# Kernel optimization log

Hardware: AMD Instinct MI355X
Metric: run time of the kernel (lower is better)

The kernel has to match this reference:

```python
import jax, jax.numpy as jnp
import numpy as np

D = 512      # model dim
H = 8        # heads
HD = D // H  # head dim = 64
NQ = 2048    # n_query
NC = 4096    # n_context
EPS = 1e-5   # LayerNorm eps (torch default)


def setup_inputs() -> dict:
    key = jax.random.key(0)
    ks = jax.random.split(key, 12)
    s = 0.02
    return {
        "query_repr": jax.random.normal(ks[0], (NQ, D), dtype=jnp.float32),
        "context_repr": jax.random.normal(ks[1], (NC, D), dtype=jnp.float32),
        "query_coords": jax.random.uniform(ks[2], (NQ, 2), dtype=jnp.float32) * 10.0,
        "context_coords": jax.random.uniform(ks[3], (NC, 2), dtype=jnp.float32) * 10.0,
        "Wq": jax.random.normal(ks[4], (D, D), dtype=jnp.float32) * s,
        "bq": jnp.zeros((D,), jnp.float32),
        "Wk": jax.random.normal(ks[5], (D, D), dtype=jnp.float32) * s,
        "bk": jnp.zeros((D,), jnp.float32),
        "Wv": jax.random.normal(ks[6], (D, D), dtype=jnp.float32) * s,
        "bv": jnp.zeros((D,), jnp.float32),
        "Wo": jax.random.normal(ks[7], (D, D), dtype=jnp.float32) * s,
        "bo": jnp.zeros((D,), jnp.float32),
        "ln_g": jnp.ones((D,), jnp.float32),
        "ln_b": jnp.zeros((D,), jnp.float32),
        "log_scale": jnp.array(0.0, jnp.float32),          # log_distance_scale
        "bias_per_head": jnp.ones((H,), jnp.float32),      # distance_bias_per_head
    }


def reference(query_repr, context_repr, query_coords, context_coords,
              Wq, bq, Wk, bk, Wv, bv, Wo, bo, ln_g, ln_b,
              log_scale, bias_per_head):
    # pairwise Euclidean distances (NQ, NC)
    diff = query_coords[:, None, :] - context_coords[None, :, :]
    dist = jnp.sqrt(jnp.sum(diff * diff, axis=-1))
    # per-head additive attention bias (H, NQ, NC)
    bias = (-jnp.exp(log_scale) * dist)[None, :, :] * bias_per_head[:, None, None]

    # multi-head attention (batch=1, eval mode so dropout is identity)
    q = (query_repr @ Wq.T + bq).reshape(NQ, H, HD).transpose(1, 0, 2)    # (H, NQ, HD)
    k = (context_repr @ Wk.T + bk).reshape(NC, H, HD).transpose(1, 0, 2)  # (H, NC, HD)
    v = (context_repr @ Wv.T + bv).reshape(NC, H, HD).transpose(1, 0, 2)  # (H, NC, HD)

    scale = 1.0 / jnp.sqrt(jnp.float32(HD))
    scores = jnp.einsum('hqd,hkd->hqk', q, k) * scale + bias              # (H, NQ, NC)
    attn = jax.nn.softmax(scores, axis=-1)
    ctx = jnp.einsum('hqk,hkd->hqd', attn, v)                             # (H, NQ, HD)
    attended = ctx.transpose(1, 0, 2).reshape(NQ, D) @ Wo.T + bo          # (NQ, D)

    # residual + LayerNorm
    x = attended + query_repr
    mu = jnp.mean(x, axis=-1, keepdims=True)
    var = jnp.mean((x - mu) ** 2, axis=-1, keepdims=True)
    return (x - mu) / jnp.sqrt(var + EPS) * ln_g + ln_b
```

## Files before the change

### kernel.cpp

```cpp
#include <hip/hip_runtime.h>

#define D 512
#define H 8
#define HD 64
#define NQ 2048
#define NC 4096
#define SPLIT 8
#define CLEN (NC / SPLIT)
#define NT (CLEN / 32)
#define M0 3.0f
#define KP2 136
#define VP 40

typedef __attribute__((ext_vector_type(8))) short short8;
typedef __attribute__((ext_vector_type(4))) short short4v;
typedef __attribute__((ext_vector_type(4))) float float4v;
typedef __attribute__((ext_vector_type(4))) int int4v;

__device__ inline float bf2f(short s) {
    unsigned int u = ((unsigned int)(unsigned short)s) << 16;
    return __builtin_bit_cast(float, u);
}
__device__ inline short f2bf(float f) {
    unsigned int u = __builtin_bit_cast(unsigned int, f);
    u = (u + 0x7FFF + ((u >> 16) & 1)) >> 16;
    return (short)u;
}
__device__ inline int cvtpk(float a, float b) {
    int w;
    asm("v_cvt_pk_bf16_f32 %0, %1, %2" : "=v"(w) : "v"(a), "v"(b));
    return w;
}

__global__ __launch_bounds__(256) void cast_all(
    const float* __restrict__ s0, const float* __restrict__ s1,
    const float* __restrict__ s2, const float* __restrict__ s3,
    const float* __restrict__ s4, const float* __restrict__ s5,
    short* __restrict__ dst)
{
    int i = blockIdx.x * 256 + threadIdx.x;
    const float* src; int off;
    if      (i < 262144) { src = s0; off = i; }
    else if (i < 786432) { src = s1; off = i - 262144; }
    else if (i < 851968) { src = s2; off = i - 786432; }
    else if (i < 917504) { src = s3; off = i - 851968; }
    else if (i < 983040) { src = s4; off = i - 917504; }
    else                 { src = s5; off = i - 983040; }
    float4v v = ((const float4v*)src)[off];
    short4v o;
    o.x = f2bf(v.x); o.y = f2bf(v.y); o.z = f2bf(v.z); o.w = f2bf(v.w);
    ((short4v*)dst)[i] = o;
}

__global__ __launch_bounds__(256) void gemm_bt_bias(
    const short* __restrict__ X, const short* __restrict__ W,
    const float* __restrict__ bias, short* __restrict__ out, int M)
{
    int wave = threadIdx.x >> 6, lane = threadIdx.x & 63;
    int gt = blockIdx.x * 4 + wave;
    int tm = gt >> 3;
    int tg = gt & 7;
    if (tm >= (M >> 4)) return;
    int l15 = lane & 15, quad = lane >> 4;
    const short* xp = X + (tm * 16 + l15) * D + quad * 8;
    const short* wp = W + (tg * 64 + l15) * D + quad * 8;
    float4v a0 = {0,0,0,0}, a1 = {0,0,0,0}, a2 = {0,0,0,0}, a3 = {0,0,0,0};
#pragma unroll
    for (int k = 0; k < D; k += 32) {
        short8 a  = *(const short8*)(xp + k);
        short8 b0 = *(const short8*)(wp + k);
        short8 b1 = *(const short8*)(wp + 16 * D + k);
        short8 b2 = *(const short8*)(wp + 32 * D + k);
        short8 b3 = *(const short8*)(wp + 48 * D + k);
        a0 = __builtin_amdgcn_mfma_f32_16x16x32_bf16(a, b0, a0, 0, 0, 0);
        a1 = __builtin_amdgcn_mfma_f32_16x16x32_bf16(a, b1, a1, 0, 0, 0);
        a2 = __builtin_amdgcn_mfma_f32_16x16x32_bf16(a, b2, a2, 0, 0, 0);
        a3 = __builtin_amdgcn_mfma_f32_16x16x32_bf16(a, b3, a3, 0, 0, 0);
    }
    int orow = tm * 16 + quad * 4;
    float4v accs[4] = {a0, a1, a2, a3};
#pragma unroll
    for (int j = 0; j < 4; j++) {
        int col = tg * 64 + j * 16 + l15;
        float bv = bias[col];
#pragma unroll
        for (int r = 0; r < 4; r++)
            out[(orow + r) * D + col] = f2bf(accs[j][r] + bv);
    }
}

__global__ __launch_bounds__(256) void gemm_bt_bias_kv(
    const short* __restrict__ X, const short* __restrict__ Wk,
    const short* __restrict__ Wv, const float* __restrict__ bk,
    const float* __restrict__ bv, short* __restrict__ outK,
    short* __restrict__ outVT, int M)
{
    int wave = threadIdx.x >> 6, lane = threadIdx.x & 63;
    int gt = blockIdx.x * 4 + wave;
    int tm = gt >> 3;
    int tg = gt & 7;
    if (tm >= (M >> 4)) return;
    int l15 = lane & 15, quad = lane >> 4;
    const short* xp  = X  + (tm * 16 + l15) * D + quad * 8;
    const short* wkp = Wk + (tg * 64 + l15) * D + quad * 8;
    const short* wvp = Wv + (tg * 64 + l15) * D + quad * 8;
    float4v k0 = {0,0,0,0}, k1 = {0,0,0,0}, k2 = {0,0,0,0}, k3 = {0,0,0,0};
    float4v v0 = {0,0,0,0}, v1 = {0,0,0,0}, v2 = {0,0,0,0}, v3 = {0,0,0,0};
#pragma unroll
    for (int k = 0; k < D; k += 32) {
        short8 a   = *(const short8*)(xp + k);
        short8 bk0 = *(const short8*)(wkp + k);
        short8 bk1 = *(const short8*)(wkp + 16 * D + k);
        short8 bk2 = *(const short8*)(wkp + 32 * D + k);
        short8 bk3 = *(const short8*)(wkp + 48 * D + k);
        short8 bv0 = *(const short8*)(wvp + k);
        short8 bv1 = *(const short8*)(wvp + 16 * D + k);
        short8 bv2 = *(const short8*)(wvp + 32 * D + k);
        short8 bv3 = *(const short8*)(wvp + 48 * D + k);
        k0 = __builtin_amdgcn_mfma_f32_16x16x32_bf16(a, bk0, k0, 0, 0, 0);
        k1 = __builtin_amdgcn_mfma_f32_16x16x32_bf16(a, bk1, k1, 0, 0, 0);
        k2 = __builtin_amdgcn_mfma_f32_16x16x32_bf16(a, bk2, k2, 0, 0, 0);
        k3 = __builtin_amdgcn_mfma_f32_16x16x32_bf16(a, bk3, k3, 0, 0, 0);
        v0 = __builtin_amdgcn_mfma_f32_16x16x32_bf16(a, bv0, v0, 0, 0, 0);
        v1 = __builtin_amdgcn_mfma_f32_16x16x32_bf16(a, bv1, v1, 0, 0, 0);
        v2 = __builtin_amdgcn_mfma_f32_16x16x32_bf16(a, bv2, v2, 0, 0, 0);
        v3 = __builtin_amdgcn_mfma_f32_16x16x32_bf16(a, bv3, v3, 0, 0, 0);
    }
    int orow = tm * 16 + quad * 4;
    {
        float4v accs[4] = {k0, k1, k2, k3};
#pragma unroll
        for (int j = 0; j < 4; j++) {
            int col = tg * 64 + j * 16 + l15;
            float bb = bk[col];
#pragma unroll
            for (int r = 0; r < 4; r++)
                outK[(orow + r) * D + col] = f2bf(accs[j][r] + bb);
        }
    }
    {
        int a = (orow & 31) >> 2;
        int posb = (a < 4) ? (8 * a) : (8 * (a - 4) + 4);
        int cp = (orow & ~31) + posb;
        float4v accs[4] = {v0, v1, v2, v3};
#pragma unroll
        for (int j = 0; j < 4; j++) {
            int col = tg * 64 + j * 16 + l15;
            float bb = bv[col];
            short4v o;
#pragma unroll
            for (int r = 0; r < 4; r++) o[r] = f2bf(accs[j][r] + bb);
            *(short4v*)(outVT + (size_t)col * M + cp) = o;
        }
    }
}

__global__ __launch_bounds__(256) void gemm_bt_bias_res_f32(
    const short* __restrict__ X, const short* __restrict__ W,
    const float* __restrict__ bias, const float* __restrict__ resid,
    float* __restrict__ out, int M)
{
    int wave = threadIdx.x >> 6, lane = threadIdx.x & 63;
    int gt = blockIdx.x * 4 + wave;
    int tm = gt >> 3;
    int tg = gt & 7;
    if (tm >= (M >> 4)) return;
    int l15 = lane & 15, quad = lane >> 4;
    const short* xp = X + (tm * 16 + l15) * D + quad * 8;
    const short* wp = W + (tg * 64 + l15) * D + quad * 8;
    float4v a0 = {0,0,0,0}, a1 = {0,0,0,0}, a2 = {0,0,0,0}, a3 = {0,0,0,0};
#pragma unroll
    for (int k = 0; k < D; k += 32) {
        short8 a  = *(const short8*)(xp + k);
        short8 b0 = *(const short8*)(wp + k);
        short8 b1 = *(const short8*)(wp + 16 * D + k);
        short8 b2 = *(const short8*)(wp + 32 * D + k);
        short8 b3 = *(const short8*)(wp + 48 * D + k);
        a0 = __builtin_amdgcn_mfma_f32_16x16x32_bf16(a, b0, a0, 0, 0, 0);
        a1 = __builtin_amdgcn_mfma_f32_16x16x32_bf16(a, b1, a1, 0, 0, 0);
        a2 = __builtin_amdgcn_mfma_f32_16x16x32_bf16(a, b2, a2, 0, 0, 0);
        a3 = __builtin_amdgcn_mfma_f32_16x16x32_bf16(a, b3, a3, 0, 0, 0);
    }
    int orow = tm * 16 + quad * 4;
    float4v accs[4] = {a0, a1, a2, a3};
#pragma unroll
    for (int j = 0; j < 4; j++) {
        int col = tg * 64 + j * 16 + l15;
        float bv = bias[col];
#pragma unroll
        for (int r = 0; r < 4; r++) {
            int q = orow + r;
            out[q * D + col] = accs[j][r] + bv + resid[q * D + col];
        }
    }
}

__global__ __launch_bounds__(256) void attn_mfma_split9(
    const short* __restrict__ Q, const short* __restrict__ K,
    const short* __restrict__ Vp,
    const float* __restrict__ qc, const float* __restrict__ cc,
    const float* __restrict__ log_scale, const float* __restrict__ bph,
    short* __restrict__ Opart, float* __restrict__ Lpart)
{
    __shared__ __align__(16) short Klds[2][32 * KP2];
    __shared__ __align__(16) short Vlds[2][128 * VP];
    __shared__ __align__(16) float ccl[512];

    int tid = threadIdx.x;
    int wave = tid >> 6, lane = tid & 63;
    int h0 = blockIdx.y * 2;
    int sp = blockIdx.z;
    int q0 = blockIdx.x * 64 + wave * 16;
    int quad = lane >> 4, l15 = lane & 15;
    int cbase = sp * CLEN;

    const float LOG2E = 1.4426950408889634f;
    const float escale = 0.125f * LOG2E;
    const float M0L = M0 * LOG2E;
    float ebase = __expf(log_scale[0]);
    float bh0 = ebase * bph[h0] * LOG2E;
    float bh1 = ebase * bph[h0 + 1] * LOG2E;

    const short* qp = Q + (q0 + l15) * D + h0 * HD + quad * 8;
    short8 qa0_0 = *(const short8*)(qp);
    short8 qa1_0 = *(const short8*)(qp + 32);
    short8 qa0_1 = *(const short8*)(qp + 64);
    short8 qa1_1 = *(const short8*)(qp + 96);

    float qx = qc[(q0 + l15) * 2];
    float qy = qc[(q0 + l15) * 2 + 1];

    float lacc0 = 0.f, lacc1 = 0.f;
    float4v O00 = {0,0,0,0}, O01 = {0,0,0,0}, O02 = {0,0,0,0}, O03 = {0,0,0,0};
    float4v O10 = {0,0,0,0}, O11 = {0,0,0,0}, O12 = {0,0,0,0}, O13 = {0,0,0,0};

    int kr_ = tid >> 3, kc_ = tid & 7;
    int vr_ = tid >> 2, vc_ = tid & 3;
    const short* kg  = K + (size_t)h0 * HD + kc_ * 8;
    const short* vg0 = Vp + (size_t)(h0 * HD + vr_) * NC + vc_ * 8;
    const short* vg1 = Vp + (size_t)(h0 * HD + 64 + vr_) * NC + vc_ * 8;
    short* kw0a = &Klds[0][kr_ * KP2 + kc_ * 8];
    short* kw1a = &Klds[1][kr_ * KP2 + kc_ * 8];
    short* vw0a = &Vlds[0][vr_ * VP + vc_ * 8];
    short* vw0b = &Vlds[0][(64 + vr_) * VP + vc_ * 8];
    short* vw1a = &Vlds[1][vr_ * VP + vc_ * 8];
    short* vw1b = &Vlds[1][(64 + vr_) * VP + vc_ * 8];

    short8 rka, rkb, rva, rvb;

#define LOADR(c0_)                                                             \
    {                                                                          \
        const short* kp_ = kg + (size_t)((c0_) + kr_) * D;                     \
        rka = *(const short8*)(kp_);                                           \
        rkb = *(const short8*)(kp_ + 64);                                      \
        rva = *(const short8*)(vg0 + (c0_));                                   \
        rvb = *(const short8*)(vg1 + (c0_));                                   \
    }

#define DSW0 { *(short8*)kw0a = rka; *(short8*)(kw0a + 64) = rkb;              \
               *(short8*)vw0a = rva; *(short8*)vw0b = rvb; }
#define DSW1 { *(short8*)kw1a = rka; *(short8*)(kw1a + 64) = rkb;              \
               *(short8*)vw1a = rva; *(short8*)vw1b = rvb; }

    const float2* ccp = (const float2*)ccl;

#define HEAD(hoff, QA0, QA1, BH, LACC, OA, OB, OC, OD)                         \
    {                                                                          \
        short8 k00 = *(const short8*)(kb + l15 * KP2 + (hoff) + quad * 8);     \
        short8 k01 = *(const short8*)(kb + l15 * KP2 + (hoff) + 32 + quad * 8);\
        short8 k10 = *(const short8*)(kb + (16 + l15) * KP2 + (hoff) + quad * 8);\
        short8 k11 = *(const short8*)(kb + (16 + l15) * KP2 + (hoff) + 32 + quad * 8);\
        float4v s0 = {0,0,0,0}, s1 = {0,0,0,0};                                \
        s0 = __builtin_amdgcn_mfma_f32_16x16x32_bf16(k00, QA0, s0, 0, 0, 0);   \
        s0 = __builtin_amdgcn_mfma_f32_16x16x32_bf16(k01, QA1, s0, 0, 0, 0);   \
        s1 = __builtin_amdgcn_mfma_f32_16x16x32_bf16(k10, QA0, s1, 0, 0, 0);   \
        s1 = __builtin_amdgcn_mfma_f32_16x16x32_bf16(k11, QA1, s1, 0, 0, 0);   \
        short8 v0 = *(const short8*)(vb + ((hoff) / 64 * 64 + l15) * VP + quad * 8);       \
        short8 v1 = *(const short8*)(vb + ((hoff) / 64 * 64 + 16 + l15) * VP + quad * 8);  \
        short8 v2 = *(const short8*)(vb + ((hoff) / 64 * 64 + 32 + l15) * VP + quad * 8);  \
        short8 v3 = *(const short8*)(vb + ((hoff) / 64 * 64 + 48 + l15) * VP + quad * 8);  \
        float p00 = exp2f(__fmaf_rn(s0[0], escale, __fmaf_rn(-(BH), dA0, -M0L)));\
        float p01 = exp2f(__fmaf_rn(s0[1], escale, __fmaf_rn(-(BH), dA1, -M0L)));\
        float p02 = exp2f(__fmaf_rn(s0[2], escale, __fmaf_rn(-(BH), dA2, -M0L)));\
        float p03 = exp2f(__fmaf_rn(s0[3], escale, __fmaf_rn(-(BH), dA3, -M0L)));\
        float p10 = exp2f(__fmaf_rn(s1[0], escale, __fmaf_rn(-(BH), dB0, -M0L)));\
        float p11 = exp2f(__fmaf_rn(s1[1], escale, __fmaf_rn(-(BH), dB1, -M0L)));\
        float p12 = exp2f(__fmaf_rn(s1[2], escale, __fmaf_rn(-(BH), dB2, -M0L)));\
        float p13 = exp2f(__fmaf_rn(s1[3], escale, __fmaf_rn(-(BH), dB3, -M0L)));\
        LACC += ((p00 + p01) + (p02 + p03)) + ((p10 + p11) + (p12 + p13));     \
        int4v pw;                                                              \
        pw.x = cvtpk(p00, p01); pw.y = cvtpk(p02, p03);                        \
        pw.z = cvtpk(p10, p11); pw.w = cvtpk(p12, p13);                        \
        short8 pa = __builtin_bit_cast(short8, pw);                            \
        OA = __builtin_amdgcn_mfma_f32_16x16x32_bf16(pa, v0, OA, 0, 0, 0);     \
        OB = __builtin_amdgcn_mfma_f32_16x16x32_bf16(pa, v1, OB, 0, 0, 0);     \
        OC = __builtin_amdgcn_mfma_f32_16x16x32_bf16(pa, v2, OC, 0, 0, 0);     \
        OD = __builtin_amdgcn_mfma_f32_16x16x32_bf16(pa, v3, OD, 0, 0, 0);     \
    }

#define COMPUTE_TILE(B, lo)                                                    \
    {                                                                          \
        const short* kb = &Klds[B][0];                                         \
        const short* vb = &Vlds[B][0];                                         \
        float2 ca0 = ccp[(lo) + 4 * quad + 0], cb0 = ccp[(lo) + 16 + 4 * quad + 0];\
        float2 ca1 = ccp[(lo) + 4 * quad + 1], cb1 = ccp[(lo) + 16 + 4 * quad + 1];\
        float2 ca2 = ccp[(lo) + 4 * quad + 2], cb2 = ccp[(lo) + 16 + 4 * quad + 2];\
        float2 ca3 = ccp[(lo) + 4 * quad + 3], cb3 = ccp[(lo) + 16 + 4 * quad + 3];\
        float dx, dy;                                                          \
        dx = qx - ca0.x; dy = qy - ca0.y;                                      \
        float dA0 = __builtin_amdgcn_sqrtf(__fmaf_rn(dx, dx, dy * dy));        \
        dx = qx - ca1.x; dy = qy - ca1.y;                                      \
        float dA1 = __builtin_amdgcn_sqrtf(__fmaf_rn(dx, dx, dy * dy));        \
        dx = qx - ca2.x; dy = qy - ca2.y;                                      \
        float dA2 = __builtin_amdgcn_sqrtf(__fmaf_rn(dx, dx, dy * dy));        \
        dx = qx - ca3.x; dy = qy - ca3.y;                                      \
        float dA3 = __builtin_amdgcn_sqrtf(__fmaf_rn(dx, dx, dy * dy));        \
        dx = qx - cb0.x; dy = qy - cb0.y;                                      \
        float dB0 = __builtin_amdgcn_sqrtf(__fmaf_rn(dx, dx, dy * dy));        \
        dx = qx - cb1.x; dy = qy - cb1.y;                                      \
        float dB1 = __builtin_amdgcn_sqrtf(__fmaf_rn(dx, dx, dy * dy));        \
        dx = qx - cb2.x; dy = qy - cb2.y;                                      \
        float dB2 = __builtin_amdgcn_sqrtf(__fmaf_rn(dx, dx, dy * dy));        \
        dx = qx - cb3.x; dy = qy - cb3.y;                                      \
        float dB3 = __builtin_amdgcn_sqrtf(__fmaf_rn(dx, dx, dy * dy));        \
        HEAD(0,  qa0_0, qa1_0, bh0, lacc0, O00, O01, O02, O03)                 \
        HEAD(64, qa0_1, qa1_1, bh1, lacc1, O10, O11, O12, O13)                 \
    }

    ((float2*)ccl)[tid] = ((const float2*)cc)[cbase + tid];
    LOADR(cbase);
    DSW0;
    LOADR(cbase + 32);
    __syncthreads();

    for (int t = 0; t < NT - 2; t += 2) {
        int c0 = cbase + t * 32;
        if (t == 8) {
            ((float2*)ccl)[tid] = ((const float2*)cc)[cbase + 256 + tid];
            __syncthreads();
        }
        DSW1;
        LOADR(c0 + 64);
        COMPUTE_TILE(0, (t & 7) * 32);
        __syncthreads();
        DSW0;
        LOADR(c0 + 96);
        COMPUTE_TILE(1, (t & 7) * 32 + 32);
        __syncthreads();
    }
    DSW1;
    COMPUTE_TILE(0, 192);
    __syncthreads();
    COMPUTE_TILE(1, 224);

#undef LOADR
#undef DSW0
#undef DSW1
#undef HEAD
#undef COMPUTE_TILE

    lacc0 += __shfl_xor(lacc0, 16);
    lacc0 += __shfl_xor(lacc0, 32);
    lacc1 += __shfl_xor(lacc1, 16);
    lacc1 += __shfl_xor(lacc1, 32);

    long base0 = (long)(sp * H + h0) * NQ;
    long base1 = base0 + NQ;
    float4v Oarr0[4] = {O00, O01, O02, O03};
    float4v Oarr1[4] = {O10, O11, O12, O13};
#pragma unroll
    for (int t = 0; t < 4; t++) {
#pragma unroll
        for (int r = 0; r < 4; r++) {
            int q = q0 + quad * 4 + r;
            Opart[(base0 + q) * HD + t * 16 + l15] = f2bf(Oarr0[t][r]);
            Opart[(base1 + q) * HD + t * 16 + l15] = f2bf(Oarr1[t][r]);
        }
    }
    if (lane < 16) {
        Lpart[base0 + q0 + lane] = lacc0;
        Lpart[base1 + q0 + lane] = lacc1;
    }
}

__global__ __launch_bounds__(256) void attn_combine(
    const short* __restrict__ Opart, const float* __restrict__ Lpart,
    short* __restrict__ Att)
{
    int id = blockIdx.x * 256 + threadIdx.x;
    int d = id & 63;
    int q = (id >> 6) & (NQ - 1);
    int h = id >> 17;
    float L = 0.f, acc = 0.f;
#pragma unroll
    for (int s = 0; s < SPLIT; s++) {
        long b = (long)(s * H + h) * NQ + q;
        L   += Lpart[b];
        acc += bf2f(Opart[b * HD + d]);
    }
    Att[q * D + h * HD + d] = f2bf(acc / L);
}

__global__ __launch_bounds__(256) void attn_mfma(
    const short* __restrict__ Q, const short* __restrict__ K,
    const short* __restrict__ V,
    const float* __restrict__ qc, const float* __restrict__ cc,
    const float* __restrict__ log_scale, const float* __restrict__ bph,
    short* __restrict__ out)
{
    __shared__ short Vt[HD][48];
    __shared__ short P[4][16][48];
    int wave = threadIdx.x >> 6, lane = threadIdx.x & 63;
    int h = blockIdx.y;
    int q0 = blockIdx.x * 64 + wave * 16;
    int quad = lane >> 4, l15 = lane & 15;
    const float scale = 0.125f;
    float bh = __expf(log_scale[0]) * bph[h];
    const short* qp = Q + (q0 + l15) * D + h * HD + quad * 8;
    short8 qa0 = *(const short8*)(qp);
    short8 qa1 = *(const short8*)(qp + 32);
    float qx[4], qy[4];
#pragma unroll
    for (int r = 0; r < 4; r++) {
        int q = q0 + quad * 4 + r;
        qx[r] = qc[q * 2]; qy[r] = qc[q * 2 + 1];
    }
    float m[4], l[4];
    float4v O[4];
#pragma unroll
    for (int r = 0; r < 4; r++) { m[r] = -1e30f; l[r] = 0.f; }
#pragma unroll
    for (int t = 0; t < 4; t++) O[t] = (float4v){0.f, 0.f, 0.f, 0.f};
    for (int c0 = 0; c0 < NC; c0 += 32) {
        __syncthreads();
        {
            int c = threadIdx.x >> 3;
            int dblk = (threadIdx.x & 7) * 8;
            short8 vv = *(const short8*)(V + (c0 + c) * D + h * HD + dblk);
#pragma unroll
            for (int j = 0; j < 8; j++) Vt[dblk + j][c] = vv[j];
        }
        const short* kp0 = K + (c0 + l15) * D + h * HD + quad * 8;
        const short* kp1 = kp0 + 16 * D;
        short8 kb00 = *(const short8*)(kp0);
        short8 kb01 = *(const short8*)(kp0 + 32);
        short8 kb10 = *(const short8*)(kp1);
        short8 kb11 = *(const short8*)(kp1 + 32);
        float4v s0 = {0,0,0,0}, s1 = {0,0,0,0};
        s0 = __builtin_amdgcn_mfma_f32_16x16x32_bf16(qa0, kb00, s0, 0, 0, 0);
        s0 = __builtin_amdgcn_mfma_f32_16x16x32_bf16(qa1, kb01, s0, 0, 0, 0);
        s1 = __builtin_amdgcn_mfma_f32_16x16x32_bf16(qa0, kb10, s1, 0, 0, 0);
        s1 = __builtin_amdgcn_mfma_f32_16x16x32_bf16(qa1, kb11, s1, 0, 0, 0);
        int cA = c0 + l15, cB = cA + 16;
        float cxA = cc[cA * 2], cyA = cc[cA * 2 + 1];
        float cxB = cc[cB * 2], cyB = cc[cB * 2 + 1];
#pragma unroll
        for (int r = 0; r < 4; r++) {
            float dxA = qx[r] - cxA, dyA = qy[r] - cyA;
            float dxB = qx[r] - cxB, dyB = qy[r] - cyB;
            float v0 = s0[r] * scale - bh * sqrtf(dxA * dxA + dyA * dyA);
            float v1 = s1[r] * scale - bh * sqrtf(dxB * dxB + dyB * dyB);
            float mx = fmaxf(v0, v1);
#pragma unroll
            for (int off = 1; off < 16; off <<= 1) mx = fmaxf(mx, __shfl_xor(mx, off));
            float mnew = fmaxf(m[r], mx);
            float alpha = __expf(m[r] - mnew);
            float p0 = __expf(v0 - mnew);
            float p1 = __expf(v1 - mnew);
            float ps = p0 + p1;
#pragma unroll
            for (int off = 1; off < 16; off <<= 1) ps += __shfl_xor(ps, off);
            l[r] = l[r] * alpha + ps;
            m[r] = mnew;
#pragma unroll
            for (int t = 0; t < 4; t++) O[t][r] *= alpha;
            P[wave][quad * 4 + r][l15]      = f2bf(p0);
            P[wave][quad * 4 + r][16 + l15] = f2bf(p1);
        }
        __syncthreads();
        short8 pa = *(const short8*)(&P[wave][l15][quad * 8]);
#pragma unroll
        for (int t = 0; t < 4; t++) {
            short8 vb = *(const short8*)(&Vt[t * 16 + l15][quad * 8]);
            O[t] = __builtin_amdgcn_mfma_f32_16x16x32_bf16(pa, vb, O[t], 0, 0, 0);
        }
    }
#pragma unroll
    for (int t = 0; t < 4; t++) {
#pragma unroll
        for (int r = 0; r < 4; r++) {
            int q = q0 + quad * 4 + r;
            out[q * D + h * HD + t * 16 + l15] = f2bf(O[t][r] / l[r]);
        }
    }
}

__global__ __launch_bounds__(256) void layernorm_kernel(
    const float* __restrict__ X, const float* __restrict__ g,
    const float* __restrict__ b, float* __restrict__ out)
{
    int wave = threadIdx.x >> 6, lane = threadIdx.x & 63;
    int row = blockIdx.x * 4 + wave;
    const float* xp = X + row * D;
    float v[8];
    float s = 0.f;
#pragma unroll
    for (int i = 0; i < 8; i++) { v[i] = xp[lane + i * 64]; s += v[i]; }
#pragma unroll
    for (int off = 1; off < 64; off <<= 1) s += __shfl_xor(s, off);
    float mu = s * (1.f / D);
    float var = 0.f;
#pragma unroll
    for (int i = 0; i < 8; i++) { float d = v[i] - mu; var += d * d; }
#pragma unroll
    for (int off = 1; off < 64; off <<= 1) var += __shfl_xor(var, off);
    float rstd = rsqrtf(var * (1.f / D) + 1e-5f);
#pragma unroll
    for (int i = 0; i < 8; i++) {
        int c = lane + i * 64;
        out[row * D + c] = (v[i] - mu) * rstd * g[c] + b[c];
    }
}

extern "C" void kernel_launch(void* const* d_in, const int* in_sizes, int n_in,
                              void* d_out, int out_size, void* d_ws, size_t ws_size,
                              hipStream_t stream) {
    const float* query_repr     = (const float*)d_in[0];
    const float* context_repr   = (const float*)d_in[1];
    const float* query_coords   = (const float*)d_in[2];
    const float* context_coords = (const float*)d_in[3];
    const float* Wq = (const float*)d_in[4];
    const float* bq = (const float*)d_in[5];
    const float* Wk = (const float*)d_in[6];
    const float* bk = (const float*)d_in[7];
    const float* Wv = (const float*)d_in[8];
    const float* bv = (const float*)d_in[9];
    const float* Wo = (const float*)d_in[10];
    const float* bo = (const float*)d_in[11];
    const float* ln_g = (const float*)d_in[12];
    const float* ln_b = (const float*)d_in[13];
    const float* log_scale = (const float*)d_in[14];
    const float* bph = (const float*)d_in[15];

    short* ws = (short*)d_ws;
    short* Xq_bf = ws;
    short* Xc_bf = Xq_bf + NQ * D;
    short* Wq_bf = Xc_bf + NC * D;
    short* Wk_bf = Wq_bf + D * D;
    short* Wv_bf = Wk_bf + D * D;
    short* Wo_bf = Wv_bf + D * D;
    short* Qw  = Wo_bf + D * D;
    short* Kw  = Qw + NQ * D;
    short* Vw  = Kw + NC * D;
    short* Att = Vw + NC * D;
    float* Xf  = (float*)(Att + NQ * D);
    short* Opart = (short*)(Xf + NQ * D);
    float* Lpart = (float*)(Opart + (size_t)SPLIT * H * NQ * HD);
    size_t ws_needed_split = ((char*)(Lpart + (size_t)SPLIT * H * NQ)) - (char*)d_ws;

    cast_all<<<dim3(4096), 256, 0, stream>>>(
        query_repr, context_repr, Wq, Wk, Wv, Wo, Xq_bf);

    gemm_bt_bias<<<dim3((NQ / 16) * 8 / 4), 256, 0, stream>>>(Xq_bf, Wq_bf, bq, Qw, NQ);

    if (ws_size >= ws_needed_split) {
        gemm_bt_bias_kv<<<dim3((NC / 16) * 8 / 4), 256, 0, stream>>>(
            Xc_bf, Wk_bf, Wv_bf, bk, bv, Kw, Vw, NC);
        attn_mfma_split9<<<dim3(NQ / 64, H / 2, SPLIT), 256, 0, stream>>>(
            Qw, Kw, Vw, query_coords, context_coords, log_scale, bph,
            Opart, Lpart);
        attn_combine<<<dim3(H * NQ * HD / 256), 256, 0, stream>>>(
            Opart, Lpart, Att);
    } else {
        gemm_bt_bias<<<dim3((NC / 16) * 8 / 4), 256, 0, stream>>>(
            Xc_bf, Wk_bf, bk, Kw, NC);
        gemm_bt_bias<<<dim3((NC / 16) * 8 / 4), 256, 0, stream>>>(
            Xc_bf, Wv_bf, bv, Vw, NC);
        attn_mfma<<<dim3(NQ / 64, H), 256, 0, stream>>>(
            Qw, Kw, Vw, query_coords, context_coords, log_scale, bph, Att);
    }

    gemm_bt_bias_res_f32<<<dim3((NQ / 16) * 8 / 4), 256, 0, stream>>>(
        Att, Wo_bf, bo, query_repr, Xf, NQ);

    layernorm_kernel<<<dim3(NQ / 4), 256, 0, stream>>>(Xf, ln_g, ln_b, (float*)d_out);
}
```

Before: 200.4 us.

## Merge Q/KV projections into one launch and fuse output GEMM with LayerNorm

The Q projection and the K/V projection now run in a single kernel launch, with blocks split by index. This removes one launch and lets the two GEMMs fill the GPU together. The output projection is fused with the residual add and LayerNorm: each block computes a full 16-row by 512-column tile and reduces mean and variance through shared memory. That avoids writing and re-reading the fp32 intermediate and a separate LayerNorm launch. The cost is fewer blocks for the output GEMM (128 instead of 256) and more accumulator registers per wave.

```diff
diff --git a/kernel.cpp b/kernel.cpp
--- a/kernel.cpp
+++ b/kernel.cpp
@@ -89,68 +89,213 @@
     }
 }
 
-__global__ __launch_bounds__(256) void gemm_bt_bias_kv(
-    const short* __restrict__ X, const short* __restrict__ Wk,
-    const short* __restrict__ Wv, const float* __restrict__ bk,
-    const float* __restrict__ bv, short* __restrict__ outK,
-    short* __restrict__ outVT, int M)
+__global__ __launch_bounds__(256) void gemm_qkv(
+    const short* __restrict__ Xq, const short* __restrict__ Xc,
+    const short* __restrict__ Wq, const short* __restrict__ Wk,
+    const short* __restrict__ Wv,
+    const float* __restrict__ bq, const float* __restrict__ bk,
+    const float* __restrict__ bv,
+    short* __restrict__ Qout, short* __restrict__ Kout,
+    short* __restrict__ VoutT)
 {
     int wave = threadIdx.x >> 6, lane = threadIdx.x & 63;
-    int gt = blockIdx.x * 4 + wave;
-    int tm = gt >> 3;
-    int tg = gt & 7;
-    if (tm >= (M >> 4)) return;
     int l15 = lane & 15, quad = lane >> 4;
-    const short* xp  = X  + (tm * 16 + l15) * D + quad * 8;
-    const short* wkp = Wk + (tg * 64 + l15) * D + quad * 8;
-    const short* wvp = Wv + (tg * 64 + l15) * D + quad * 8;
-    float4v k0 = {0,0,0,0}, k1 = {0,0,0,0}, k2 = {0,0,0,0}, k3 = {0,0,0,0};
-    float4v v0 = {0,0,0,0}, v1 = {0,0,0,0}, v2 = {0,0,0,0}, v3 = {0,0,0,0};
+    int blk = blockIdx.x;
+    if (blk < 256) {
+        int gt = blk * 4 + wave;
+        int tm = gt >> 3, tg = gt & 7;
+        const short* xp = Xq + (tm * 16 + l15) * D + quad * 8;
+        const short* wp = Wq + (tg * 64 + l15) * D + quad * 8;
+        float4v a0 = {0,0,0,0}, a1 = {0,0,0,0}, a2 = {0,0,0,0}, a3 = {0,0,0,0};
+#pragma unroll
+        for (int k = 0; k < D; k += 32) {
+            short8 a  = *(const short8*)(xp + k);
+            short8 b0 = *(const short8*)(wp + k);
+            short8 b1 = *(const short8*)(wp + 16 * D + k);
+            short8 b2 = *(const short8*)(wp + 32 * D + k);
+            short8 b3 = *(const short8*)(wp + 48 * D + k);
+            a0 = __builtin_amdgcn_mfma_f32_16x16x32_bf16(a, b0, a0, 0, 0, 0);
+            a1 = __builtin_amdgcn_mfma_f32_16x16x32_bf16(a, b1, a1, 0, 0, 0);
+            a2 = __builtin_amdgcn_mfma_f32_16x16x32_bf16(a, b2, a2, 0, 0, 0);
+            a3 = __builtin_amdgcn_mfma_f32_16x16x32_bf16(a, b3, a3, 0, 0, 0);
+        }
+        int orow = tm * 16 + quad * 4;
+        float4v accs[4] = {a0, a1, a2, a3};
+#pragma unroll
+        for (int j = 0; j < 4; j++) {
+            int col = tg * 64 + j * 16 + l15;
+            float bb = bq[col];
+#pragma unroll
+            for (int r = 0; r < 4; r++)
+                Qout[(orow + r) * D + col] = f2bf(accs[j][r] + bb);
+        }
+    } else {
+        int gt = (blk - 256) * 4 + wave;
+        int tm = gt >> 3, tg = gt & 7;
+        const short* xp  = Xc + (tm * 16 + l15) * D + quad * 8;
+        const short* wkp = Wk + (tg * 64 + l15) * D + quad * 8;
+        const short* wvp = Wv + (tg * 64 + l15) * D + quad * 8;
+        float4v k0 = {0,0,0,0}, k1 = {0,0,0,0}, k2 = {0,0,0,0}, k3 = {0,0,0,0};
+        float4v v0 = {0,0,0,0}, v1 = {0,0,0,0}, v2 = {0,0,0,0}, v3 = {0,0,0,0};
+#pragma unroll
+        for (int k = 0; k < D; k += 32) {
+            short8 a   = *(const short8*)(xp + k);
+            short8 bk0 = *(const short8*)(wkp + k);
+            short8 bk1 = *(const short8*)(wkp + 16 * D + k);
+            short8 bk2 = *(const short8*)(wkp + 32 * D + k);
+            short8 bk3 = *(const short8*)(wkp + 48 * D + k);
+            short8 bv0 = *(const short8*)(wvp + k);
+            short8 bv1 = *(const short8*)(wvp + 16 * D + k);
+            short8 bv2 = *(const short8*)(wvp + 32 * D + k);
+            short8 bv3 = *(const short8*)(wvp + 48 * D + k);
+            k0 = __builtin_amdgcn_mfma_f32_16x16x32_bf16(a, bk0, k0, 0, 0, 0);
+            k1 = __builtin_amdgcn_mfma_f32_16x16x32_bf16(a, bk1, k1, 0, 0, 0);
+            k2 = __builtin_amdgcn_mfma_f32_16x16x32_bf16(a, bk2, k2, 0, 0, 0);
+            k3 = __builtin_amdgcn_mfma_f32_16x16x32_bf16(a, bk3, k3, 0, 0, 0);
+            v0 = __builtin_amdgcn_mfma_f32_16x16x32_bf16(a, bv0, v0, 0, 0, 0);
+            v1 = __builtin_amdgcn_mfma_f32_16x16x32_bf16(a, bv1, v1, 0, 0, 0);
+            v2 = __builtin_amdgcn_mfma_f32_16x16x32_bf16(a, bv2, v2, 0, 0, 0);
+            v3 = __builtin_amdgcn_mfma_f32_16x16x32_bf16(a, bv3, v3, 0, 0, 0);
+        }
+        int orow = tm * 16 + quad * 4;
+        {
+            float4v accs[4] = {k0, k1, k2, k3};
+#pragma unroll
+            for (int j = 0; j < 4; j++) {
+                int col = tg * 64 + j * 16 + l15;
+                float bb = bk[col];
+#pragma unroll
+                for (int r = 0; r < 4; r++)
+                    Kout[(orow + r) * D + col] = f2bf(accs[j][r] + bb);
+            }
+        }
+        {
+            int a = (orow & 31) >> 2;
+            int posb = (a < 4) ? (8 * a) : (8 * (a - 4) + 4);
+            int cp = (orow & ~31) + posb;
+            float4v accs[4] = {v0, v1, v2, v3};
+#pragma unroll
+            for (int j = 0; j < 4; j++) {
+                int col = tg * 64 + j * 16 + l15;
+                float bb = bv[col];
+                short4v o;
+#pragma unroll
+                for (int r = 0; r < 4; r++) o[r] = f2bf(accs[j][r] + bb);
+                *(short4v*)(VoutT + (size_t)col * NC + cp) = o;
+            }
+        }
+    }
+}
+
+__global__ __launch_bounds__(256) void gemm_res_ln(
+    const short* __restrict__ X, const short* __restrict__ W,
+    const float* __restrict__ bias, const float* __restrict__ resid,
+    const float* __restrict__ g, const float* __restrict__ b,
+    float* __restrict__ out)
+{
+    __shared__ float redS[4][4][4];
+    __shared__ float redV[4][4][4];
+
+    int wave = threadIdx.x >> 6, lane = threadIdx.x & 63;
+    int l15 = lane & 15, quad = lane >> 4;
+    int tm = blockIdx.x;
+    const short* xp  = X + (tm * 16 + l15) * D + quad * 8;
+    const short* wp0 = W + ((2 * wave) * 64 + l15) * D + quad * 8;
+    const short* wp1 = wp0 + 64 * D;
+    float4v a00 = {0,0,0,0}, a01 = {0,0,0,0}, a02 = {0,0,0,0}, a03 = {0,0,0,0};
+    float4v a10 = {0,0,0,0}, a11 = {0,0,0,0}, a12 = {0,0,0,0}, a13 = {0,0,0,0};
 #pragma unroll
     for (int k = 0; k < D; k += 32) {
         short8 a   = *(const short8*)(xp + k);
-        short8 bk0 = *(const short8*)(wkp + k);
-        short8 bk1 = *(const short8*)(wkp + 16 * D + k);
-        short8 bk2 = *(const short8*)(wkp + 32 * D + k);
-        short8 bk3 = *(const short8*)(wkp + 48 * D + k);
-        short8 bv0 = *(const short8*)(wvp + k);
-        short8 bv1 = *(const short8*)(wvp + 16 * D + k);
-        short8 bv2 = *(const short8*)(wvp + 32 * D + k);
-        short8 bv3 = *(const short8*)(wvp + 48 * D + k);
-        k0 = __builtin_amdgcn_mfma_f32_16x16x32_bf16(a, bk0, k0, 0, 0, 0);
-        k1 = __builtin_amdgcn_mfma_f32_16x16x32_bf16(a, bk1, k1, 0, 0, 0);
-        k2 = __builtin_amdgcn_mfma_f32_16x16x32_bf16(a, bk2, k2, 0, 0, 0);
-        k3 = __builtin_amdgcn_mfma_f32_16x16x32_bf16(a, bk3, k3, 0, 0, 0);
-        v0 = __builtin_amdgcn_mfma_f32_16x16x32_bf16(a, bv0, v0, 0, 0, 0);
-        v1 = __builtin_amdgcn_mfma_f32_16x16x32_bf16(a, bv1, v1, 0, 0, 0);
-        v2 = __builtin_amdgcn_mfma_f32_16x16x32_bf16(a, bv2, v2, 0, 0, 0);
-        v3 = __builtin_amdgcn_mfma_f32_16x16x32_bf16(a, bv3, v3, 0, 0, 0);
+        short8 b00 = *(const short8*)(wp0 + k);
+        short8 b01 = *(const short8*)(wp0 + 16 * D + k);
+        short8 b02 = *(const short8*)(wp0 + 32 * D + k);
+        short8 b03 = *(const short8*)(wp0 + 48 * D + k);
+        short8 b10 = *(const short8*)(wp1 + k);
+        short8 b11 = *(const short8*)(wp1 + 16 * D + k);
+        short8 b12 = *(const short8*)(wp1 + 32 * D + k);
+        short8 b13 = *(const short8*)(wp1 + 48 * D + k);
+        a00 = __builtin_amdgcn_mfma_f32_16x16x32_bf16(a, b00, a00, 0, 0, 0);
+        a01 = __builtin_amdgcn_mfma_f32_16x16x32_bf16(a, b01, a01, 0, 0, 0);
+        a02 = __builtin_amdgcn_mfma_f32_16x16x32_bf16(a, b02, a02, 0, 0, 0);
+        a03 = __builtin_amdgcn_mfma_f32_16x16x32_bf16(a, b03, a03, 0, 0, 0);
+        a10 = __builtin_amdgcn_mfma_f32_16x16x32_bf16(a, b10, a10, 0, 0, 0);
+        a11 = __builtin_amdgcn_mfma_f32_16x16x32_bf16(a, b11, a11, 0, 0, 0);
+        a12 = __builtin_amdgcn_mfma_f32_16x16x32_bf16(a, b12, a12, 0, 0, 0);
+        a13 = __builtin_amdgcn_mfma_f32_16x16x32_bf16(a, b13, a13, 0, 0, 0);
     }
     int orow = tm * 16 + quad * 4;
-    {
-        float4v accs[4] = {k0, k1, k2, k3};
+    float v[2][4][4];
+    float4v accs[2][4] = {{a00, a01, a02, a03}, {a10, a11, a12, a13}};
+#pragma unroll
+    for (int t = 0; t < 2; t++) {
 #pragma unroll
         for (int j = 0; j < 4; j++) {
-            int col = tg * 64 + j * 16 + l15;
-            float bb = bk[col];
+            int col = (2 * wave + t) * 64 + j * 16 + l15;
+            float bv = bias[col];
 #pragma unroll
             for (int r = 0; r < 4; r++)
-                outK[(orow + r) * D + col] = f2bf(accs[j][r] + bb);
-        }
-    }
-    {
-        int a = (orow & 31) >> 2;
-        int posb = (a < 4) ? (8 * a) : (8 * (a - 4) + 4);
-        int cp = (orow & ~31) + posb;
-        float4v accs[4] = {v0, v1, v2, v3};
+                v[t][j][r] = accs[t][j][r] + bv + resid[(orow + r) * D + col];
+        }
+    }
+    float ps[4];
+#pragma unroll
+    for (int r = 0; r < 4; r++) {
+        float s = 0.f;
+#pragma unroll
+        for (int t = 0; t < 2; t++)
+#pragma unroll
+            for (int j = 0; j < 4; j++) s += v[t][j][r];
+#pragma unroll
+        for (int off = 1; off < 16; off <<= 1) s += __shfl_xor(s, off);
+        ps[r] = s;
+    }
+    if (l15 == 0) {
+#pragma unroll
+        for (int r = 0; r < 4; r++) redS[wave][quad][r] = ps[r];
+    }
+    __syncthreads();
+    float mu[4];
+#pragma unroll
+    for (int r = 0; r < 4; r++)
+        mu[r] = (redS[0][quad][r] + redS[1][quad][r] +
+                 redS[2][quad][r] + redS[3][quad][r]) * (1.f / D);
+#pragma unroll
+    for (int r = 0; r < 4; r++) {
+        float s = 0.f;
+#pragma unroll
+        for (int t = 0; t < 2; t++)
+#pragma unroll
+            for (int j = 0; j < 4; j++) {
+                float d = v[t][j][r] - mu[r];
+                s += d * d;
+            }
+#pragma unroll
+        for (int off = 1; off < 16; off <<= 1) s += __shfl_xor(s, off);
+        ps[r] = s;
+    }
+    if (l15 == 0) {
+#pragma unroll
+        for (int r = 0; r < 4; r++) redV[wave][quad][r] = ps[r];
+    }
+    __syncthreads();
+    float rstd[4];
+#pragma unroll
+    for (int r = 0; r < 4; r++) {
+        float var = (redV[0][quad][r] + redV[1][quad][r] +
+                     redV[2][quad][r] + redV[3][quad][r]) * (1.f / D);
+        rstd[r] = rsqrtf(var + 1e-5f);
+    }
+#pragma unroll
+    for (int t = 0; t < 2; t++) {
 #pragma unroll
         for (int j = 0; j < 4; j++) {
-            int col = tg * 64 + j * 16 + l15;
-            float bb = bv[col];
-            short4v o;
-#pragma unroll
-            for (int r = 0; r < 4; r++) o[r] = f2bf(accs[j][r] + bb);
-            *(short4v*)(outVT + (size_t)col * M + cp) = o;
+            int col = (2 * wave + t) * 64 + j * 16 + l15;
+            float gc = g[col], bc = b[col];
+#pragma unroll
+            for (int r = 0; r < 4; r++)
+                out[(orow + r) * D + col] =
+                    (v[t][j][r] - mu[r]) * rstd[r] * gc + bc;
         }
     }
 }
@@ -561,27 +706,28 @@
     cast_all<<<dim3(4096), 256, 0, stream>>>(
         query_repr, context_repr, Wq, Wk, Wv, Wo, Xq_bf);
 
-    gemm_bt_bias<<<dim3((NQ / 16) * 8 / 4), 256, 0, stream>>>(Xq_bf, Wq_bf, bq, Qw, NQ);
-
     if (ws_size >= ws_needed_split) {
-        gemm_bt_bias_kv<<<dim3((NC / 16) * 8 / 4), 256, 0, stream>>>(
-            Xc_bf, Wk_bf, Wv_bf, bk, bv, Kw, Vw, NC);
+        gemm_qkv<<<dim3(768), 256, 0, stream>>>(
+            Xq_bf, Xc_bf, Wq_bf, Wk_bf, Wv_bf, bq, bk, bv, Qw, Kw, Vw);
         attn_mfma_split9<<<dim3(NQ / 64, H / 2, SPLIT), 256, 0, stream>>>(
             Qw, Kw, Vw, query_coords, context_coords, log_scale, bph,
             Opart, Lpart);
         attn_combine<<<dim3(H * NQ * HD / 256), 256, 0, stream>>>(
             Opart, Lpart, Att);
+        gemm_res_ln<<<dim3(NQ / 16), 256, 0, stream>>>(
+            Att, Wo_bf, bo, query_repr, ln_g, ln_b, (float*)d_out);
     } else {
+        gemm_bt_bias<<<dim3((NQ / 16) * 8 / 4), 256, 0, stream>>>(
+            Xq_bf, Wq_bf, bq, Qw, NQ);
         gemm_bt_bias<<<dim3((NC / 16) * 8 / 4), 256, 0, stream>>>(
             Xc_bf, Wk_bf, bk, Kw, NC);
         gemm_bt_bias<<<dim3((NC / 16) * 8 / 4), 256, 0, stream>>>(
             Xc_bf, Wv_bf, bv, Vw, NC);
         attn_mfma<<<dim3(NQ / 64, H), 256, 0, stream>>>(
             Qw, Kw, Vw, query_coords, context_coords, log_scale, bph, Att);
-    }
-
-    gemm_bt_bias_res_f32<<<dim3((NQ / 16) * 8 / 4), 256, 0, stream>>>(
-        Att, Wo_bf, bo, query_repr, Xf, NQ);
-
-    layernorm_kernel<<<dim3(NQ / 4), 256, 0, stream>>>(Xf, ln_g, ln_b, (float*)d_out);
-}
+        gemm_bt_bias_res_f32<<<dim3((NQ / 16) * 8 / 4), 256, 0, stream>>>(
+            Att, Wo_bf, bo, query_repr, Xf, NQ);
+        layernorm_kernel<<<dim3(NQ / 4), 256, 0, stream>>>(
+            Xf, ln_g, ln_b, (float*)d_out);
+    }
+}
```

After: 202.6 us. About the same (+1.1%).
